# Kernel tuning notes

Hardware: AMD Instinct MI355X
Metric: run time of the kernel (lower is better)

Reference implementation:

```python
import jax, jax.numpy as jnp
import numpy as np

NEG_SLOPE = 0.2
EPS = 1e-08


def conv3d_same(x, w, b):
    # x: [b,c,d,h,w], w: [o,c,kd,kh,kw], stride 1, pad SAME (==pad 1 for k=3)
    y = jax.lax.conv_general_dilated(x, w, (1, 1, 1), 'SAME',
                                     dimension_numbers=('NCDHW', 'OIDHW', 'NCDHW'))
    return y + b[None, :, None, None, None]


def get_bl(frame):
    # frame: [b,3,h,w]; replicates numpy median/mean/std stats from get_BL
    x = jnp.clip(frame, 0.0, 1.0) * 255.0
    bsz = x.shape[0]
    r_med = jnp.median(x[:, 0].reshape(bsz, -1), axis=1)          # [b]
    g_mean = jnp.mean(x[:, 1], axis=(1, 2))
    g_std = jnp.std(x[:, 1], axis=(1, 2))                          # ddof=0, like np.std
    b_mean = jnp.mean(x[:, 2], axis=(1, 2))
    b_std = jnp.std(x[:, 2], axis=(1, 2))
    bl_r = 140.0 / (1.0 + 14.4 * jnp.exp(-0.034 * r_med))
    bl_g = 1.13 * g_mean + 1.11 * g_std - 25.6
    bl_b = 1.13 * b_mean + 1.11 * b_std - 25.6
    bl = jnp.stack([bl_r, bl_g, bl_b], axis=1)                     # [b,3]
    bl = jnp.clip(bl, 5.0, 250.0) / 255.0
    h, w = frame.shape[2], frame.shape[3]
    return jnp.broadcast_to(bl[:, :, None, None], (bsz, 3, h, w))


def leaky(x):
    return jnp.where(x >= 0, x, NEG_SLOPE * x)


def reference(i, j, w_bl1, b_bl1, w_bl2, b_bl2, w_t1, b_t1, w_t2, b_t2, w1, w2, t_bias):
    T = i.shape[2]
    # background light from the center frame (detached in the original)
    bl2d = jax.lax.stop_gradient(get_bl(i[:, :, T // 2]))          # [b,3,h,w]
    bl = jnp.broadcast_to(bl2d[:, :, None], i.shape)               # [b,3,T,h,w]
    j5 = jnp.broadcast_to(j[:, :, None], i.shape)                  # [b,3,T,h,w]
    # AdaptiveAvgPool3d((T,1,1)) == mean over h,w keeping frames
    diff = jnp.mean(i - j5, axis=(3, 4), keepdims=True)            # [b,3,T,1,1]
    # bl_ca: two 1x1x1 convs == channel-mixing matmuls
    h1 = leaky(jnp.einsum('bcdhw,oc->bodhw', diff, w_bl1[:, :, 0, 0, 0])
               + b_bl1[None, :, None, None, None])
    bl_diff = jax.nn.sigmoid(jnp.einsum('bcdhw,oc->bodhw', h1, w_bl2[:, :, 0, 0, 0])
                             + b_bl2[None, :, None, None, None])   # [b,3,T,1,1]
    bl = bl + w1 * bl_diff                                         # broadcast over h,w
    t3 = (i - bl) / (j5 - bl + EPS)
    x = i + w2 * t3
    h2 = leaky(conv3d_same(x, w_t1, b_t1))                         # [b,16,T,h,w]
    t = jax.nn.sigmoid(conv3d_same(h2, w_t2, b_t2)) + t_bias       # [b,1,T,h,w]
    return bl, t


def setup_inputs() -> dict:
    key = jax.random.key(0)
    ks = jax.random.split(key, 12)
    b, c, T, h, w = 4, 3, 5, 512, 512
    nf = 16
    inp = {
        'i': jax.random.uniform(ks[0], (b, c, T, h, w), dtype=jnp.float32),
        'j': jax.random.uniform(ks[1], (b, c, h, w), dtype=jnp.float32),
        'w_bl1': jax.random.normal(ks[2], (nf, 3, 1, 1, 1), dtype=jnp.float32) * 0.1,
        'b_bl1': jnp.zeros((nf,), jnp.float32),
        'w_bl2': jax.random.normal(ks[3], (3, nf, 1, 1, 1), dtype=jnp.float32) * 0.1,
        'b_bl2': jnp.zeros((3,), jnp.float32),
        'w_t1': jax.random.normal(ks[4], (nf, 3, 3, 3, 3), dtype=jnp.float32) * 0.1,
        'b_t1': jnp.zeros((nf,), jnp.float32),
        'w_t2': jax.random.normal(ks[5], (1, nf, 3, 3, 3), dtype=jnp.float32) * 0.1,
        'b_t2': jnp.zeros((1,), jnp.float32),
        'w1': jnp.zeros((1,), jnp.float32),
        'w2': jnp.zeros((1,), jnp.float32),
        't_bias': jnp.zeros((1, 1, T, 1, 1), jnp.float32),
    }
    return inp
```

## Files before the change

kernel.cpp:

```cpp
#include <hip/hip_runtime.h>

typedef unsigned int uint;
typedef unsigned short ushort;
typedef short bf16x8 __attribute__((ext_vector_type(8)));
typedef _Float16 f16x8 __attribute__((ext_vector_type(8)));
typedef float f32x4 __attribute__((ext_vector_type(4)));

#define NEG_SLOPE 0.2f

#define WS_HIST 0
#define WS_DBL  65536
#define WS_BLV  (WS_DBL + 704)
#define WS_WA   (WS_BLV + 256)
#define WS_W2A  (WS_WA + 4096)
#define WS_ZERO_BYTES (WS_DBL + 704)

#define HCH 28
#define HROW 504

__device__ __forceinline__ float leakyf(float x) { return fmaxf(x, NEG_SLOPE * x); }

__device__ __forceinline__ ushort f2bf(float f) {
  uint u = __float_as_uint(f);
  uint r = u + 0x7FFFu + ((u >> 16) & 1u);
  return (ushort)(r >> 16);
}
__device__ __forceinline__ uint cvt_pk_u32(float a, float b) {
  union { __fp16 __attribute__((ext_vector_type(2))) h; uint u; } c;
  c.h = __builtin_amdgcn_cvt_pkrtz(a, b);
  return c.u;
}

__global__ __launch_bounds__(256) void stats_kernel(const float* __restrict__ gi,
                                                    const float* __restrict__ gj,
                                                    double* __restrict__ sums,
                                                    uint* __restrict__ hist) {
  __shared__ double red[256];
  __shared__ uint lh[4096];
  const int plane = blockIdx.y;
  const int chunk = blockIdx.x;
  const int tid = threadIdx.x;

  if (plane >= 60) {
    const int jp = plane - 60;
    const float4* base = (const float4*)(gj + (size_t)jp * 262144);
    double dsum = 0.0;
    for (int k = 0; k < 8; ++k) {
      float4 v = base[chunk * 2048 + k * 256 + tid];
      dsum += (double)v.x + (double)v.y + (double)v.z + (double)v.w;
    }
    red[tid] = dsum; __syncthreads();
    for (int off = 128; off > 0; off >>= 1) { if (tid < off) red[tid] += red[tid + off]; __syncthreads(); }
    if (tid == 0) atomicAdd(&sums[60 + jp], red[0]);
    return;
  }

  const int b = plane / 15;
  const int rem = plane % 15;
  const int c = rem / 5;
  const int t = rem % 5;
  const float4* base = (const float4*)(gi + (size_t)plane * 262144);
  const bool dostat = (c >= 1 && t == 2);
  const bool domed = (c == 0 && t == 2);
  if (domed) {
    for (int i = tid; i < 4096; i += 256) lh[i] = 0;
    __syncthreads();
  }
  double dsum = 0.0, dsx = 0.0, dsx2 = 0.0;
  for (int k = 0; k < 8; ++k) {
    float4 v = base[chunk * 2048 + k * 256 + tid];
    dsum += (double)v.x + (double)v.y + (double)v.z + (double)v.w;
    if (dostat || domed) {
      float arr[4] = {v.x, v.y, v.z, v.w};
#pragma unroll
      for (int q = 0; q < 4; ++q) {
        float x = fminf(fmaxf(arr[q], 0.f), 1.f) * 255.f;
        if (domed) {
          int bin = (int)(x * (4096.0f / 255.0f));
          if (bin > 4095) bin = 4095;
          atomicAdd(&lh[bin], 1u);
        } else {
          dsx += (double)x;
          dsx2 += (double)x * (double)x;
        }
      }
    }
  }
  red[tid] = dsum; __syncthreads();
  for (int off = 128; off > 0; off >>= 1) { if (tid < off) red[tid] += red[tid + off]; __syncthreads(); }
  if (tid == 0) atomicAdd(&sums[plane], red[0]);
  __syncthreads();
  if (dostat) {
    red[tid] = dsx; __syncthreads();
    for (int off = 128; off > 0; off >>= 1) { if (tid < off) red[tid] += red[tid + off]; __syncthreads(); }
    if (tid == 0) atomicAdd(&sums[72 + b * 2 + (c - 1)], red[0]);
    __syncthreads();
    red[tid] = dsx2; __syncthreads();
    for (int off = 128; off > 0; off >>= 1) { if (tid < off) red[tid] += red[tid + off]; __syncthreads(); }
    if (tid == 0) atomicAdd(&sums[80 + b * 2 + (c - 1)], red[0]);
  }
  if (domed) {
    for (int i = tid; i < 4096; i += 256) { uint v = lh[i]; if (v) atomicAdd(&hist[b * 4096 + i], v); }
  }
}

__global__ void setup_kernel(const float* __restrict__ w_t1, const float* __restrict__ w_t2,
                             ushort* __restrict__ wA, ushort* __restrict__ w2A) {
  const int tid = threadIdx.x;
  for (int idx = tid; idx < 2048; idx += 256) {
    int o = idx >> 7, k = idx & 127, g = k >> 2, kw = k & 3;
    float v = 0.f;
    if (g < 27 && kw < 3) {
      int ci = g / 9, kd = (g % 9) / 3, kh = g % 3;
      v = w_t1[o * 81 + ci * 27 + kd * 9 + kh * 3 + kw];
    }
    wA[idx] = f2bf(v);
  }
  for (int idx = tid; idx < 12800; idx += 256) {
    int j = idx & 7;
    int lane = (idx >> 3) & 63;
    int rest = idx >> 9;
    int step = rest % 5;
    int tf = rest / 5;
    int ln = lane & 15, kb = lane >> 4;
    int k = kb * 8 + j;
    int tap = step * 2 + (k >> 4);
    int ch = k & 15;
    float v = 0.f;
    if (ln < 5 && tap < 9) {
      int kd = tf + 1 - ln;
      if (kd >= 0 && kd <= 2) v = w_t2[ch * 27 + kd * 9 + tap];
    }
    union { ushort s; _Float16 h; } cv; cv.h = (_Float16)v;
    w2A[idx] = cv.s;
  }
}

__global__ __launch_bounds__(256) void finalize_kernel(const uint* __restrict__ hist,
                                const double* __restrict__ sums,
                                const float* __restrict__ w_bl1, const float* __restrict__ b_bl1,
                                const float* __restrict__ w_bl2, const float* __restrict__ b_bl2,
                                const float* __restrict__ w1, float* __restrict__ blv) {
  __shared__ uint s[256];
  __shared__ float fv[2];
  __shared__ float rmed_s[4];
  const int tid = threadIdx.x;
  for (int b = 0; b < 4; ++b) {
    const uint* h = hist + b * 4096;
    uint loc[16]; uint part = 0;
#pragma unroll
    for (int q = 0; q < 16; ++q) { loc[q] = h[tid * 16 + q]; part += loc[q]; }
    s[tid] = part; __syncthreads();
    for (int off = 1; off < 256; off <<= 1) {
      uint v = (tid >= off) ? s[tid - off] : 0u;
      __syncthreads(); s[tid] += v; __syncthreads();
    }
    uint pref = s[tid] - part;
#pragma unroll
    for (int m = 0; m < 2; ++m) {
      uint k = 131071u + (uint)m;
      if (k >= pref && k < pref + part) {
        uint cum = pref;
        for (int q = 0; q < 16; ++q) {
          if (k < cum + loc[q]) { fv[m] = ((float)(tid * 16 + q) + 0.5f) * (255.f / 4096.f); break; }
          cum += loc[q];
        }
      }
    }
    __syncthreads();
    if (tid == 0) rmed_s[b] = 0.5f * (fv[0] + fv[1]);
    __syncthreads();
  }
  if (tid < 20) {
    const int b = tid / 5, t = tid % 5;
    const double inv = 1.0 / 262144.0;
    float bl2[3];
    bl2[0] = 140.f / (1.f + 14.4f * expf(-0.034f * rmed_s[b]));
    for (int c = 1; c < 3; ++c) {
      double m = sums[72 + b * 2 + (c - 1)] * inv;
      double ex2 = sums[80 + b * 2 + (c - 1)] * inv;
      double var = ex2 - m * m;
      if (var < 0.0) var = 0.0;
      bl2[c] = (float)(1.13 * m + 1.11 * sqrt(var) - 25.6);
    }
#pragma unroll
    for (int c = 0; c < 3; ++c)
      bl2[c] = fminf(fmaxf(bl2[c], 5.f), 250.f) * (1.f / 255.f);
    float diff[3];
    for (int c = 0; c < 3; ++c)
      diff[c] = (float)((sums[(b * 3 + c) * 5 + t] - sums[60 + b * 3 + c]) * inv);
    float h1[16];
    for (int o = 0; o < 16; ++o) {
      float sv = b_bl1[o];
      for (int c = 0; c < 3; ++c) sv += w_bl1[o * 3 + c] * diff[c];
      h1[o] = leakyf(sv);
    }
    const float w1v = w1[0];
    for (int c = 0; c < 3; ++c) {
      float sv = b_bl2[c];
      for (int o = 0; o < 16; ++o) sv += w_bl2[c * 16 + o] * h1[o];
      float sg = 1.f / (1.f + expf(-sv));
      blv[(b * 3 + c) * 5 + t] = bl2[c] + w1v * sg;
    }
  }
}

__global__ __launch_bounds__(256) void fused_kernel(
    const float* __restrict__ gi, const float* __restrict__ gj,
    const ushort* __restrict__ wAg, const float* __restrict__ b_t1,
    const ushort* __restrict__ w2Ag, const float* __restrict__ b_t2,
    const float* __restrict__ w2p, const float* __restrict__ t_bias,
    const float* __restrict__ blv, float* __restrict__ out) {
  __shared__ __align__(16) ushort xsh[10560];
  __shared__ __align__(16) ushort h2sh[324 * HCH];
  __shared__ float blv_s[15];

  const int b = blockIdx.z;
  const int lin = blockIdx.y * 32 + blockIdx.x;
  const int swz = (lin & 7) * 128 + (lin >> 3);
  const int tY = swz >> 5, tX = swz & 31;
  const int tid = threadIdx.x;
  const int wv = tid >> 6;
  const int lane = tid & 63;
  const int ln = lane & 15;
  const int kb = lane >> 4;
  const int ty = tid >> 4, tx = tid & 15;
  const int gy = tY * 16 + ty, gx = tX * 16 + tx;
  const int ybase = tY * 16 - 2, xbase = tX * 16 - 2;

  if (tid < 15) blv_s[tid] = blv[b * 15 + tid];
  for (int i = tid; i < 5280; i += 256) ((uint*)xsh)[i] = 0u;

  union { uint4 u; bf16x8 v; } a4[4];
#pragma unroll
  for (int m = 0; m < 4; ++m)
    a4[m].u = *(const uint4*)(wAg + ln * 128 + m * 32 + kb * 8);
  f32x4 bias4;
#pragma unroll
  for (int r = 0; r < 4; ++r) bias4[r] = b_t1[kb * 4 + r];

  int sbase[8], kdE[8];
#pragma unroll
  for (int e = 0; e < 8; ++e) {
    int m = e >> 1, j = e & 1;
    int g = m * 8 + kb * 2 + j;
    int ci = 0, kd = 0, kh = 0;
    if (g < 27) { ci = g / 9; kd = (g % 9) / 3; kh = g % 3; } else { kd = 99; }
    sbase[e] = ci * 440 + kh * 22;
    kdE[e] = kd;
  }

  int qT[6], hOffT[6];
  uint tmask = 0;
#pragma unroll
  for (int i = 0; i < 6; ++i) {
    int tile = wv + i * 4;
    int pos = tile * 16 + ln;
    int pe = pos < 324 ? pos : 323;
    int y0 = pe / 18, x0 = pe - y0 * 18;
    int p = x0 & 1;
    qT[i] = y0 * 22 + x0 - p + p * 5280;
    hOffT[i] = (y0 * 18 + x0) * HCH + kb * 4;
    int gyh = tY * 16 - 1 + y0, gxh = tX * 16 - 1 + x0;
    if (pos < 324) tmask |= 1u << i;
    if (gyh >= 0 && gyh < 512 && gxh >= 0 && gxh < 512) tmask |= 1u << (i + 8);
  }

  int bOff[5];
#pragma unroll
  for (int s = 0; s < 5; ++s) {
    int tap = s * 2 + (kb >> 1); if (tap > 8) tap = 8;
    int kh = tap / 3, kw = tap - kh * 3;
    bOff[s] = kh * HROW + kw * HCH + (kb & 1) * 8 + ln * HCH;
  }

  int qi5[5], eb5[5], civ5[5];
  float jv5[5];
  uint vmask = 0;
#pragma unroll
  for (int k = 0; k < 5; ++k) {
    int idx = tid + k * 256;
    int idc = idx < 1200 ? idx : 0;
    int ci = idc / 400, rem = idc - ci * 400;
    int ys = rem / 20, xx = rem - ys * 20;
    int gyy = ybase + ys, gxx = xbase + xx;
    bool inb = (idx < 1200) && gyy >= 0 && gyy < 512 && gxx >= 0 && gxx < 512;
    int cy = gyy < 0 ? 0 : (gyy > 511 ? 511 : gyy);
    int cx = gxx < 0 ? 0 : (gxx > 511 ? 511 : gxx);
    int spc = cy * 512 + cx;
    qi5[k] = (b * 3 + ci) * 1310720 + spc;
    jv5[k] = gj[(b * 3 + ci) * 262144 + spc];
    eb5[k] = ci * 440 + ys * 22 + xx;
    civ5[k] = ci * 5;
    if (inb) vmask |= 1u << k;
    if (xx > 0) vmask |= 1u << (k + 8);
  }

  const float w2v = w2p[0];

  auto issue_loads = [&](int f, float* ivr) {
    const int fo = f * 262144;
    ivr[0] = gi[qi5[0] + fo];
    ivr[1] = gi[qi5[1] + fo];
    ivr[2] = gi[qi5[2] + fo];
    ivr[3] = gi[qi5[3] + fo];
    ivr[4] = (tid < 176) ? gi[qi5[4] + fo] : 0.f;
  };
  auto stage_frame = [&](int f, const float* ivr) {
    const int slot = f % 3;
    const int sb2 = slot * 1320;
#pragma unroll
    for (int k = 0; k < 5; ++k) {
      if (k == 4 && tid >= 176) break;
      float iv = ivr[k];
      float bv = blv_s[civ5[k] + f];
      float num = iv - bv;
      float den = jv5[k] - bv + 1e-8f;
      float xv = ((vmask >> k) & 1u) ? fmaf(w2v, num * __builtin_amdgcn_rcpf(den), iv) : 0.f;
      ushort hx = f2bf(xv);
      int ebb = sb2 + eb5[k];
      xsh[ebb] = hx;
      if ((vmask >> (k + 8)) & 1u) xsh[ebb + 5279] = hx;
    }
  };

  float ivr0[5], ivr1[5];
  issue_loads(0, ivr0);
  issue_loads(1, ivr1);

  __syncthreads();

#pragma unroll
  for (int c = 0; c < 3; ++c)
#pragma unroll
    for (int t = 0; t < 5; ++t)
      out[(((b * 3 + c) * 5 + t) * 512 + gy) * 512 + gx] = blv_s[c * 5 + t];

  stage_frame(0, ivr0);
  stage_frame(1, ivr1);
  __syncthreads();

  f32x4 acc2[4];
#pragma unroll
  for (int u = 0; u < 4; ++u) acc2[u] = (f32x4){0.f, 0.f, 0.f, 0.f};

#pragma unroll
  for (int tf = 0; tf < 5; ++tf) {
    float ivr[5];
    if (tf < 3) issue_loads(tf + 2, ivr);

    union { uint4 u; f16x8 v; } aw[5];
#pragma unroll
    for (int s = 0; s < 5; ++s)
      aw[s].u = *(const uint4*)(w2Ag + ((tf * 5 + s) * 64 + lane) * 8);

    int baseE[8];
#pragma unroll
    for (int e = 0; e < 8; ++e) {
      int f = tf + kdE[e] - 1;
      int sl = (f < 0 || f > 4 || kdE[e] == 99) ? 3 : (f % 3);
      baseE[e] = sbase[e] + sl * 1320;
    }

#pragma unroll
    for (int i = 0; i < 6; ++i) {
      if (i == 5 && wv != 0) continue;
      const int q = qT[i];
      uint u0[8], u1[8];
#pragma unroll
      for (int e = 0; e < 8; ++e) {
        const uint* pu = (const uint*)(xsh + (baseE[e] + q));
        u0[e] = pu[0]; u1[e] = pu[1];
      }
      f32x4 acc = bias4;
#pragma unroll
      for (int m = 0; m < 4; ++m) {
        union { uint4 u; bf16x8 v; } bfr;
        bfr.u = make_uint4(u0[2 * m], u1[2 * m], u0[2 * m + 1], u1[2 * m + 1]);
        acc = __builtin_amdgcn_mfma_f32_16x16x32_bf16(a4[m].v, bfr.v, acc, 0, 0, 0);
      }
      const bool inimg = (tmask >> (i + 8)) & 1u;
      float r0 = inimg ? leakyf(acc[0]) : 0.f;
      float r1 = inimg ? leakyf(acc[1]) : 0.f;
      float r2 = inimg ? leakyf(acc[2]) : 0.f;
      float r3 = inimg ? leakyf(acc[3]) : 0.f;
      uint p0 = cvt_pk_u32(r0, r1);
      uint p1 = cvt_pk_u32(r2, r3);
      if ((tmask >> i) & 1u)
        *(uint2*)(h2sh + hOffT[i]) = make_uint2(p0, p1);
    }
    __syncthreads();

#pragma unroll
    for (int u = 0; u < 4; ++u) {
      const int tt = wv + u * 4;
      const ushort* hb = h2sh + tt * HROW;
#pragma unroll
      for (int s = 0; s < 5; ++s) {
        uint2 lo = *(const uint2*)(hb + bOff[s]);
        uint2 hi = *(const uint2*)(hb + bOff[s] + 4);
        union { uint4 u4; f16x8 v; } bfr;
        bfr.u4 = make_uint4(lo.x, lo.y, hi.x, hi.y);
        acc2[u] = __builtin_amdgcn_mfma_f32_16x16x32_f16(aw[s].v, bfr.v, acc2[u], 0, 0, 0);
      }
    }

    if (tf < 3) stage_frame(tf + 2, ivr);
    __syncthreads();
  }

  float* sredf = (float*)xsh;
#pragma unroll
  for (int u = 0; u < 4; ++u) {
    const int tt = wv + u * 4;
    if (kb == 0) {
#pragma unroll
      for (int r = 0; r < 4; ++r)
        sredf[r * 256 + tt * 16 + ln] = acc2[u][r];
    } else if (kb == 1) {
      sredf[4 * 256 + tt * 16 + ln] = acc2[u][0];
    }
  }
  __syncthreads();

  const float bt2 = b_t2[0];
#pragma unroll
  for (int t = 0; t < 5; ++t) {
    float tv = 1.f / (1.f + __expf(-(sredf[t * 256 + tid] + bt2))) + t_bias[t];
    out[15728640 + ((b * 5 + t) * 512 + gy) * 512 + gx] = tv;
  }
}

extern "C" void kernel_launch(void* const* d_in, const int* in_sizes, int n_in,
                              void* d_out, int out_size, void* d_ws, size_t ws_size,
                              hipStream_t stream) {
  const float* gi = (const float*)d_in[0];
  const float* gj = (const float*)d_in[1];
  const float* w_bl1 = (const float*)d_in[2];
  const float* b_bl1 = (const float*)d_in[3];
  const float* w_bl2 = (const float*)d_in[4];
  const float* b_bl2 = (const float*)d_in[5];
  const float* w_t1 = (const float*)d_in[6];
  const float* b_t1 = (const float*)d_in[7];
  const float* w_t2 = (const float*)d_in[8];
  const float* b_t2 = (const float*)d_in[9];
  const float* w1 = (const float*)d_in[10];
  const float* w2 = (const float*)d_in[11];
  const float* t_bias = (const float*)d_in[12];
  float* out = (float*)d_out;
  char* ws = (char*)d_ws;

  uint* hist = (uint*)(ws + WS_HIST);
  double* sums = (double*)(ws + WS_DBL);
  float* blv = (float*)(ws + WS_BLV);
  ushort* wA = (ushort*)(ws + WS_WA);
  ushort* w2A = (ushort*)(ws + WS_W2A);

  hipMemsetAsync(ws, 0, WS_ZERO_BYTES, stream);

  setup_kernel<<<1, 256, 0, stream>>>(w_t1, w_t2, wA, w2A);
  stats_kernel<<<dim3(32, 72), 256, 0, stream>>>(gi, gj, sums, hist);
  finalize_kernel<<<1, 256, 0, stream>>>(hist, sums, w_bl1, b_bl1, w_bl2, b_bl2, w1, blv);
  fused_kernel<<<dim3(32, 32, 4), 256, 0, stream>>>(gi, gj, wA, b_t1, w2A, b_t2, w2, t_bias, blv, out);
}
```

Before: 178.1 us.

## Fold temporal boundary zeros into per-frame conv1 weights to shrink LDS

The first 3D conv weights are now prepared per output frame, with taps that fall outside the valid frame range zeroed. This removes the need for a fourth all-zero slot in the staged input buffer, and those taps now read slot 0 instead. The x staging buffer and the h2 channel stride (HCH 28 to 20) both shrink, cutting LDS per block and possibly allowing more resident blocks. The cost is a weight fragment reload from global memory every frame instead of once per block, plus a smaller padded stride that could raise LDS bank conflicts.

After: 197.1 us. 10.6% more time.

```diff
diff --git a/kernel.cpp b/kernel.cpp
--- a/kernel.cpp
+++ b/kernel.cpp
@@ -12,11 +12,14 @@
 #define WS_DBL  65536
 #define WS_BLV  (WS_DBL + 704)
 #define WS_WA   (WS_BLV + 256)
-#define WS_W2A  (WS_WA + 4096)
+#define WS_W2A  (WS_WA + 20480)
 #define WS_ZERO_BYTES (WS_DBL + 704)
 
-#define HCH 28
-#define HROW 504
+#define XSLOT 1320
+#define XCOPY 3960
+#define XTOT  7920
+#define HCH 20
+#define HROW 360
 
 __device__ __forceinline__ float leakyf(float x) { return fmaxf(x, NEG_SLOPE * x); }
 
@@ -105,16 +108,20 @@
 }
 
 __global__ void setup_kernel(const float* __restrict__ w_t1, const float* __restrict__ w_t2,
-                             ushort* __restrict__ wA, ushort* __restrict__ w2A) {
+                             ushort* __restrict__ wA5, ushort* __restrict__ w2A) {
   const int tid = threadIdx.x;
-  for (int idx = tid; idx < 2048; idx += 256) {
-    int o = idx >> 7, k = idx & 127, g = k >> 2, kw = k & 3;
+  for (int idx = tid; idx < 10240; idx += 256) {
+    int tf = idx >> 11;
+    int r = idx & 2047;
+    int o = r >> 7, k = r & 127, g = k >> 2, kw = k & 3;
     float v = 0.f;
     if (g < 27 && kw < 3) {
       int ci = g / 9, kd = (g % 9) / 3, kh = g % 3;
-      v = w_t1[o * 81 + ci * 27 + kd * 9 + kh * 3 + kw];
-    }
-    wA[idx] = f2bf(v);
+      int f = tf + kd - 1;
+      if (f >= 0 && f <= 4)
+        v = w_t1[o * 81 + ci * 27 + kd * 9 + kh * 3 + kw];
+    }
+    wA5[idx] = f2bf(v);
   }
   for (int idx = tid; idx < 12800; idx += 256) {
     int j = idx & 7;
@@ -207,11 +214,11 @@
 
 __global__ __launch_bounds__(256) void fused_kernel(
     const float* __restrict__ gi, const float* __restrict__ gj,
-    const ushort* __restrict__ wAg, const float* __restrict__ b_t1,
+    const ushort* __restrict__ wA5, const float* __restrict__ b_t1,
     const ushort* __restrict__ w2Ag, const float* __restrict__ b_t2,
     const float* __restrict__ w2p, const float* __restrict__ t_bias,
     const float* __restrict__ blv, float* __restrict__ out) {
-  __shared__ __align__(16) ushort xsh[10560];
+  __shared__ __align__(16) ushort xsh[XTOT];
   __shared__ __align__(16) ushort h2sh[324 * HCH];
   __shared__ float blv_s[15];
 
@@ -229,12 +236,8 @@
   const int ybase = tY * 16 - 2, xbase = tX * 16 - 2;
 
   if (tid < 15) blv_s[tid] = blv[b * 15 + tid];
-  for (int i = tid; i < 5280; i += 256) ((uint*)xsh)[i] = 0u;
-
-  union { uint4 u; bf16x8 v; } a4[4];
-#pragma unroll
-  for (int m = 0; m < 4; ++m)
-    a4[m].u = *(const uint4*)(wAg + ln * 128 + m * 32 + kb * 8);
+  for (int i = tid; i < XTOT / 2; i += 256) ((uint*)xsh)[i] = 0u;
+
   f32x4 bias4;
 #pragma unroll
   for (int r = 0; r < 4; ++r) bias4[r] = b_t1[kb * 4 + r];
@@ -259,7 +262,7 @@
     int pe = pos < 324 ? pos : 323;
     int y0 = pe / 18, x0 = pe - y0 * 18;
     int p = x0 & 1;
-    qT[i] = y0 * 22 + x0 - p + p * 5280;
+    qT[i] = y0 * 22 + x0 - p + p * XCOPY;
     hOffT[i] = (y0 * 18 + x0) * HCH + kb * 4;
     int gyh = tY * 16 - 1 + y0, gxh = tX * 16 - 1 + x0;
     if (pos < 324) tmask |= 1u << i;
@@ -308,7 +311,7 @@
   };
   auto stage_frame = [&](int f, const float* ivr) {
     const int slot = f % 3;
-    const int sb2 = slot * 1320;
+    const int sb2 = slot * XSLOT;
 #pragma unroll
     for (int k = 0; k < 5; ++k) {
       if (k == 4 && tid >= 176) break;
@@ -320,7 +323,7 @@
       ushort hx = f2bf(xv);
       int ebb = sb2 + eb5[k];
       xsh[ebb] = hx;
-      if ((vmask >> (k + 8)) & 1u) xsh[ebb + 5279] = hx;
+      if ((vmask >> (k + 8)) & 1u) xsh[ebb + XCOPY - 1] = hx;
     }
   };
 
@@ -349,6 +352,10 @@
     float ivr[5];
     if (tf < 3) issue_loads(tf + 2, ivr);
 
+    union { uint4 u; bf16x8 v; } a4[4];
+#pragma unroll
+    for (int m = 0; m < 4; ++m)
+      a4[m].u = *(const uint4*)(wA5 + tf * 2048 + ln * 128 + m * 32 + kb * 8);
     union { uint4 u; f16x8 v; } aw[5];
 #pragma unroll
     for (int s = 0; s < 5; ++s)
@@ -358,8 +365,8 @@
 #pragma unroll
     for (int e = 0; e < 8; ++e) {
       int f = tf + kdE[e] - 1;
-      int sl = (f < 0 || f > 4 || kdE[e] == 99) ? 3 : (f % 3);
-      baseE[e] = sbase[e] + sl * 1320;
+      int sl = (f < 0 || f > 4 || kdE[e] == 99) ? 0 : (f % 3);
+      baseE[e] = sbase[e] + sl * XSLOT;
     }
 
 #pragma unroll
@@ -453,13 +460,13 @@
   uint* hist = (uint*)(ws + WS_HIST);
   double* sums = (double*)(ws + WS_DBL);
   float* blv = (float*)(ws + WS_BLV);
-  ushort* wA = (ushort*)(ws + WS_WA);
+  ushort* wA5 = (ushort*)(ws + WS_WA);
   ushort* w2A = (ushort*)(ws + WS_W2A);
 
   hipMemsetAsync(ws, 0, WS_ZERO_BYTES, stream);
 
-  setup_kernel<<<1, 256, 0, stream>>>(w_t1, w_t2, wA, w2A);
+  setup_kernel<<<1, 256, 0, stream>>>(w_t1, w_t2, wA5, w2A);
   stats_kernel<<<dim3(32, 72), 256, 0, stream>>>(gi, gj, sums, hist);
   finalize_kernel<<<1, 256, 0, stream>>>(hist, sums, w_bl1, b_bl1, w_bl2, b_bl2, w1, blv);
-  fused_kernel<<<dim3(32, 32, 4), 256, 0, stream>>>(gi, gj, wA, b_t1, w2A, b_t2, w2, t_bias, blv, out);
-}
+  fused_kernel<<<dim3(32, 32, 4), 256, 0, stream>>>(gi, gj, wA5, b_t1, w2A, b_t2, w2, t_bias, blv, out);
+}
```
